# Kernel optimization log

Measured on AMD Instinct MI355X. Metric: run time of the kernel, lower is better.

## Reference

```python
import jax, jax.numpy as jnp
import numpy as np

B, N, M, K, C = 4, 8192, 2048, 32, 64
RADIUS = 0.4
XYZ_OUT = 16  # xyz_mlps spec [3, 16]


def _mlp1(x, W, b):
    # SharedMLP layer: 1x1 Conv2d + ReLU (bn=False -> bias=True)
    return jax.nn.relu(jnp.einsum('oi,bimk->bomk', W, x) + b[None, :, None, None])


def _ball_query(xyz, new_xyz):
    # xyz: [B,N,3], new_xyz: [B,M,3] -> idx [B,M,K] int32, idn [B,M,K] {0,1}
    d2 = jnp.sum((new_xyz[:, :, None, :] - xyz[:, None, :, :]) ** 2, axis=-1)  # [B,M,N]
    within = d2 < RADIUS * RADIUS
    score = jnp.where(within, jnp.arange(N, dtype=jnp.int32), jnp.int32(N))
    neg, _ = jax.lax.top_k(-score, K)  # first K in-ball indices (ascending)
    idx = -neg
    valid = idx < N
    idx = jnp.where(valid, idx, idx[..., :1])  # pad with first neighbor (CUDA ball_query semantics)
    idx = jnp.clip(idx, 0, N - 1)
    return idx, valid.astype(jnp.int32)


def setup_inputs() -> dict:
    key = jax.random.key(0)
    ks = jax.random.split(key, 16)
    s = 0.1
    return {
        'xyz': jax.random.uniform(ks[0], (B, N, 3), jnp.float32),
        'new_xyz': jax.random.uniform(ks[1], (B, M, 3), jnp.float32),
        'features': jax.random.normal(ks[2], (B, C, N), jnp.float32),
        'query_features': jax.random.normal(ks[3], (B, C, M), jnp.float32),
        # query_feats_mlps[0]: [query_ch -> neigh_ch]
        'qW': s * jax.random.normal(ks[4], (C, C), jnp.float32),
        'qb': jnp.zeros((C,), jnp.float32),
        # ad_feats_mlps[0]: [neigh_ch -> neigh_ch]
        'afW': s * jax.random.normal(ks[5], (C, C), jnp.float32),
        'afb': jnp.zeros((C,), jnp.float32),
        # ad_xyz_mlps[0]: [3 -> neigh_ch]
        'axW': s * jax.random.normal(ks[6], (C, 3), jnp.float32),
        'axb': jnp.zeros((C,), jnp.float32),
        # mlps[0]: [64 -> 64 -> 64]
        'mW1': s * jax.random.normal(ks[7], (C, C), jnp.float32),
        'mb1': jnp.zeros((C,), jnp.float32),
        'mW2': s * jax.random.normal(ks[8], (C, C), jnp.float32),
        'mb2': jnp.zeros((C,), jnp.float32),
        # xyz_mlps[0]: [3 -> 16]
        'xW': s * jax.random.normal(ks[9], (XYZ_OUT, 3), jnp.float32),
        'xb': jnp.zeros((XYZ_OUT,), jnp.float32),
    }


def reference(xyz, new_xyz, features, query_features,
              qW, qb, afW, afb, axW, axb, mW1, mb1, mW2, mb2, xW, xb):
    idx, idn = _ball_query(xyz, new_xyz)  # [B,M,K]

    # gather neighbor xyz and features
    flat = idx.reshape(B, M * K)
    g_xyz = jnp.take_along_axis(xyz, flat[:, :, None], axis=1).reshape(B, M, K, 3)
    g_xyz = (g_xyz - new_xyz[:, :, None, :]).transpose(0, 3, 1, 2)  # [B,3,M,K] relative coords
    g_feat = jnp.take_along_axis(features, flat[:, None, :], axis=2).reshape(B, C, M, K)

    idn_mask = (jnp.sum(idn, axis=2) > 0).astype(jnp.float32)[:, :, None]  # [B,M,1]
    # _idn: rows with at least one neighbor keep idn, empty rows become all-ones
    _idn = jnp.where(idn_mask > 0, idn.astype(jnp.float32), 1.0)[:, None, :, :]  # [B,1,M,K]

    q = _mlp1(query_features[:, :, :, None], qW, qb)  # [B,C,M,1]

    feats_dist = _mlp1(q - g_feat, afW, afb)          # [B,C,M,K]
    space_dist = _mlp1(g_xyz, axW, axb)               # [B,C,M,K]
    bi_edge = feats_dist * space_dist

    dist = jnp.linalg.norm(g_xyz, axis=1, keepdims=True)  # [B,1,M,K]
    dist_recip = 1.0 / (dist + 1e-8)
    dist_recip = dist_recip / _idn
    norm = jnp.sum(dist_recip, axis=3, keepdims=True)
    weights = dist_recip / norm
    weights = weights * idn_mask[:, None, :, :]  # [B,1,M,K] * [B,1,M,1]

    nf = _mlp1(_mlp1(g_feat, mW1, mb1), mW2, mb2)  # [B,C,M,K]
    nf = weights * nf * bi_edge
    nf = jnp.sum(nf, axis=3)  # [B,C,M]

    nx = _mlp1(g_xyz, xW, xb)        # [B,16,M,K]
    nx = jnp.max(nx, axis=3)         # max_pool over neighbors -> [B,16,M]

    out = jnp.concatenate([nx, nf], axis=1)  # [B,80,M]
    return (new_xyz, out)
```

## Files before the change

### kernel.cpp

```cpp
#include <hip/hip_runtime.h>

#define B_ 4
#define N_ 8192
#define M_ 2048
#define K_ 32
#define R2 0.16f

__global__ __launch_bounds__(256) void pointprep(const float* __restrict__ feats,
                                                 const float* __restrict__ afW,
                                                 const float* __restrict__ mW1, const float* __restrict__ mb1,
                                                 const float* __restrict__ mW2, const float* __restrict__ mb2,
                                                 float* __restrict__ PA,
                                                 float* __restrict__ P2) {
  __shared__ float xt[64][65];
  __shared__ float x2[64][65];
  int b = blockIdx.y, p0 = blockIdx.x * 64;
  int t = threadIdx.x, lane = t & 63;
  int g = __builtin_amdgcn_readfirstlane(t >> 6);
  const float* src = feats + ((size_t)b * 64 + g * 16) * N_ + p0 + lane;
#pragma unroll
  for (int cc = 0; cc < 16; ++cc)
    xt[g * 16 + cc][lane] = src[(size_t)cc * N_];
  __syncthreads();
  size_t orow = ((size_t)b * N_ + p0 + lane) * 64 + g * 16;
  {
    float acc[16];
#pragma unroll
    for (int cc = 0; cc < 16; ++cc) acc[cc] = 0.0f;
#pragma unroll 4
    for (int i = 0; i < 64; ++i) {
      float xv = xt[i][lane];
#pragma unroll
      for (int cc = 0; cc < 16; ++cc) acc[cc] = fmaf(afW[(g * 16 + cc) * 64 + i], xv, acc[cc]);
    }
    float4* o = (float4*)(PA + orow);
#pragma unroll
    for (int q = 0; q < 4; ++q)
      o[q] = make_float4(acc[4 * q], acc[4 * q + 1], acc[4 * q + 2], acc[4 * q + 3]);
  }
  {
    float acc[16];
#pragma unroll
    for (int cc = 0; cc < 16; ++cc) acc[cc] = mb1[g * 16 + cc];
#pragma unroll 4
    for (int i = 0; i < 64; ++i) {
      float xv = xt[i][lane];
#pragma unroll
      for (int cc = 0; cc < 16; ++cc) acc[cc] = fmaf(mW1[(g * 16 + cc) * 64 + i], xv, acc[cc]);
    }
#pragma unroll
    for (int cc = 0; cc < 16; ++cc) x2[g * 16 + cc][lane] = fmaxf(acc[cc], 0.0f);
  }
  __syncthreads();
  {
    float acc[16];
#pragma unroll
    for (int cc = 0; cc < 16; ++cc) acc[cc] = mb2[g * 16 + cc];
#pragma unroll 4
    for (int i = 0; i < 64; ++i) {
      float xv = x2[i][lane];
#pragma unroll
      for (int cc = 0; cc < 16; ++cc) acc[cc] = fmaf(mW2[(g * 16 + cc) * 64 + i], xv, acc[cc]);
    }
    float4* o = (float4*)(P2 + orow);
#pragma unroll
    for (int q = 0; q < 4; ++q)
      o[q] = make_float4(fmaxf(acc[4 * q], 0.0f), fmaxf(acc[4 * q + 1], 0.0f),
                         fmaxf(acc[4 * q + 2], 0.0f), fmaxf(acc[4 * q + 3], 0.0f));
  }
}

__global__ __launch_bounds__(256) void queryprep(const float* __restrict__ qfeat,
                                                 const float* __restrict__ qW, const float* __restrict__ qb,
                                                 const float* __restrict__ afW, const float* __restrict__ afb,
                                                 const float* __restrict__ new_xyz,
                                                 float* __restrict__ QA,
                                                 float* __restrict__ outhead) {
  __shared__ float xt[64][65];
  __shared__ float x2[64][65];
  int b = blockIdx.y, p0 = blockIdx.x * 64;
  int t = threadIdx.x, lane = t & 63;
  int g = __builtin_amdgcn_readfirstlane(t >> 6);
  const float* src = qfeat + ((size_t)b * 64 + g * 16) * M_ + p0 + lane;
#pragma unroll
  for (int cc = 0; cc < 16; ++cc)
    xt[g * 16 + cc][lane] = src[(size_t)cc * M_];
  if (t < 192) {
    size_t o = (size_t)(b * M_ + p0) * 3 + t;
    outhead[o] = new_xyz[o];
  }
  __syncthreads();
  {
    float acc[16];
#pragma unroll
    for (int cc = 0; cc < 16; ++cc) acc[cc] = qb[g * 16 + cc];
#pragma unroll 4
    for (int i = 0; i < 64; ++i) {
      float xv = xt[i][lane];
#pragma unroll
      for (int cc = 0; cc < 16; ++cc) acc[cc] = fmaf(qW[(g * 16 + cc) * 64 + i], xv, acc[cc]);
    }
#pragma unroll
    for (int cc = 0; cc < 16; ++cc) x2[g * 16 + cc][lane] = fmaxf(acc[cc], 0.0f);
  }
  __syncthreads();
  {
    float acc[16];
#pragma unroll
    for (int cc = 0; cc < 16; ++cc) acc[cc] = afb[g * 16 + cc];
#pragma unroll 4
    for (int i = 0; i < 64; ++i) {
      float xv = x2[i][lane];
#pragma unroll
      for (int cc = 0; cc < 16; ++cc) acc[cc] = fmaf(afW[(g * 16 + cc) * 64 + i], xv, acc[cc]);
    }
    float4* o = (float4*)(QA + ((size_t)b * M_ + p0 + lane) * 64 + g * 16);
#pragma unroll
    for (int q = 0; q < 4; ++q)
      o[q] = make_float4(acc[4 * q], acc[4 * q + 1], acc[4 * q + 2], acc[4 * q + 3]);
  }
}

__global__ __launch_bounds__(256) void grouper_main(
    const float* __restrict__ xyz, const float* __restrict__ new_xyz,
    const float* __restrict__ PA, const float* __restrict__ P2,
    const float* __restrict__ QA,
    const float* __restrict__ axW, const float* __restrict__ axb,
    const float* __restrict__ xW, const float* __restrict__ xb,
    float* __restrict__ out) {
  int wid = (int)((blockIdx.x * (size_t)blockDim.x + threadIdx.x) >> 6);
  int lane = threadIdx.x & 63;
  int b = wid >> 11;
  int m = wid & (M_ - 1);
  const float* qc = new_xyz + ((size_t)b * M_ + m) * 3;
  float cx = qc[0], cy = qc[1], cz = qc[2];
  const float* xbp = xyz + (size_t)b * N_ * 3;

  int idxreg = N_ - 1;
  float gxr = 0.f, gyr = 0.f, gzr = 0.f, d2r = 0.f;
  int cnt = 0;
  for (int base = 0; base < N_; base += 64) {
    int n = base + lane;
    const float* pp = xbp + 3 * n;
    float dx = pp[0] - cx, dy = pp[1] - cy, dz = pp[2] - cz;
    float d2 = dx * dx + dy * dy + dz * dz;
    bool inball = d2 < R2;
    unsigned long long mask = __ballot(inball);
    int pop = __popcll(mask);
    int before = __builtin_amdgcn_mbcnt_hi((unsigned)(mask >> 32),
                 __builtin_amdgcn_mbcnt_lo((unsigned)mask, 0));
    int pos = cnt + before;
    bool push = inball && (pos < K_);
    int dest = (push ? pos : 63) << 2;
    int rI = __builtin_amdgcn_ds_permute(dest, n);
    int rX = __builtin_amdgcn_ds_permute(dest, __float_as_int(dx));
    int rY = __builtin_amdgcn_ds_permute(dest, __float_as_int(dy));
    int rZ = __builtin_amdgcn_ds_permute(dest, __float_as_int(dz));
    int rD = __builtin_amdgcn_ds_permute(dest, __float_as_int(d2));
    int newcnt = cnt + pop;
    if ((lane >= cnt) && (lane < min(newcnt, K_))) {
      idxreg = rI; gxr = __int_as_float(rX); gyr = __int_as_float(rY);
      gzr = __int_as_float(rZ); d2r = __int_as_float(rD);
    }
    cnt = newcnt;
    if (cnt >= K_) break;
  }
  int nneigh = min(cnt, K_);
  if (nneigh == 0) {
    const float* pp = xbp + 3 * (N_ - 1);
    float dx = pp[0] - cx, dy = pp[1] - cy, dz = pp[2] - cz;
    if (lane == 0) {
      idxreg = N_ - 1; gxr = dx; gyr = dy; gzr = dz;
      d2r = dx * dx + dy * dy + dz * dz;
    }
  }
  int padn = max(nneigh, 1);
  {
    int i0 = __shfl(idxreg, 0);
    float x0 = __shfl(gxr, 0), y0 = __shfl(gyr, 0), z0 = __shfl(gzr, 0), d0 = __shfl(d2r, 0);
    if (lane >= padn) { idxreg = i0; gxr = x0; gyr = y0; gzr = z0; d2r = d0; }
  }
  float idn_mask = (nneigh > 0) ? 1.0f : 0.0f;

  size_t qb64 = ((size_t)b * M_ + m) * 64;
  float QAm = QA[qb64 + lane];
  float ax0 = axW[lane * 3 + 0], ax1 = axW[lane * 3 + 1], ax2 = axW[lane * 3 + 2];
  float axbv = axb[lane];
  float xw0 = 0.f, xw1 = 0.f, xw2 = 0.f, xbv = 0.f;
  if (lane < 16) { xw0 = xW[lane * 3 + 0]; xw1 = xW[lane * 3 + 1]; xw2 = xW[lane * 3 + 2]; xbv = xb[lane]; }

  const float* PAb = PA + (size_t)b * N_ * 64;
  const float* P2b = P2 + (size_t)b * N_ * 64;

  float accS = 0.f, Rsum = 0.f, nxmax = 0.f;
#pragma unroll 8
  for (int k = 0; k < K_; ++k) {
    int n = __builtin_amdgcn_readlane(idxreg, k);
    float gx = __int_as_float(__builtin_amdgcn_readlane(__float_as_int(gxr), k));
    float gy = __int_as_float(__builtin_amdgcn_readlane(__float_as_int(gyr), k));
    float gz = __int_as_float(__builtin_amdgcn_readlane(__float_as_int(gzr), k));
    float d2 = __int_as_float(__builtin_amdgcn_readlane(__float_as_int(d2r), k));
    float pa = PAb[(size_t)n * 64 + lane];
    float h2 = P2b[(size_t)n * 64 + lane];
    float dist = __builtin_amdgcn_sqrtf(d2);
    float r = __builtin_amdgcn_rcpf(dist + 1e-8f);
    float fd = fmaxf(QAm - pa, 0.f);
    float sd = fmaxf(fmaf(ax0, gx, fmaf(ax1, gy, fmaf(ax2, gz, axbv))), 0.f);
    accS = fmaf(r, h2 * fd * sd, accS);
    Rsum += r;
    float v = fmaxf(fmaf(xw0, gx, fmaf(xw1, gy, fmaf(xw2, gz, xbv))), 0.f);
    nxmax = fmaxf(nxmax, v);
  }
  float nf = (accS / Rsum) * idn_mask;
  float* ob = out + (size_t)b * 80 * M_;
  ob[(size_t)(16 + lane) * M_ + m] = nf;
  if (lane < 16) ob[(size_t)lane * M_ + m] = nxmax;
}

extern "C" void kernel_launch(void* const* d_in, const int* in_sizes, int n_in,
                              void* d_out, int out_size, void* d_ws, size_t ws_size,
                              hipStream_t stream) {
  const float* xyz   = (const float*)d_in[0];
  const float* nxyz  = (const float*)d_in[1];
  const float* feats = (const float*)d_in[2];
  const float* qfeat = (const float*)d_in[3];
  const float* qW  = (const float*)d_in[4];
  const float* qb  = (const float*)d_in[5];
  const float* afW = (const float*)d_in[6];
  const float* afb = (const float*)d_in[7];
  const float* axW = (const float*)d_in[8];
  const float* axb = (const float*)d_in[9];
  const float* mW1 = (const float*)d_in[10];
  const float* mb1 = (const float*)d_in[11];
  const float* mW2 = (const float*)d_in[12];
  const float* mb2 = (const float*)d_in[13];
  const float* xW  = (const float*)d_in[14];
  const float* xb  = (const float*)d_in[15];

  float* ws = (float*)d_ws;
  size_t off = 0;
  float* PA = ws + off; off += (size_t)B_ * N_ * 64;
  float* P2 = ws + off; off += (size_t)B_ * N_ * 64;
  float* QA = ws + off; off += (size_t)B_ * M_ * 64;
  if (ws_size < off * sizeof(float)) return;

  pointprep<<<dim3(N_ / 64, B_), 256, 0, stream>>>(feats, afW, mW1, mb1, mW2, mb2, PA, P2);

  float* outhead = (float*)d_out;
  queryprep<<<dim3(M_ / 64, B_), 256, 0, stream>>>(qfeat, qW, qb, afW, afb, nxyz, QA, outhead);

  float* out_main = (float*)d_out + (size_t)B_ * M_ * 3;
  grouper_main<<<B_ * M_ / 4, 256, 0, stream>>>(xyz, nxyz, PA, P2, QA,
                                                axW, axb, xW, xb, out_main);
}
```

Measured before the change: 154.3 us.

## Interleave point features, merge prep kernels, and batch neighbor gathers

```diff
diff --git a/kernel.cpp b/kernel.cpp
--- a/kernel.cpp
+++ b/kernel.cpp
@@ -6,125 +6,116 @@
 #define K_ 32
 #define R2 0.16f
 
-__global__ __launch_bounds__(256) void pointprep(const float* __restrict__ feats,
-                                                 const float* __restrict__ afW,
-                                                 const float* __restrict__ mW1, const float* __restrict__ mb1,
-                                                 const float* __restrict__ mW2, const float* __restrict__ mb2,
-                                                 float* __restrict__ PA,
-                                                 float* __restrict__ P2) {
+__device__ __forceinline__ float readlane_f(float v, int k) {
+  return __int_as_float(__builtin_amdgcn_readlane(__float_as_int(v), k));
+}
+
+__global__ __launch_bounds__(256) void prep(
+    const float* __restrict__ feats, const float* __restrict__ qfeat,
+    const float* __restrict__ qW, const float* __restrict__ qb,
+    const float* __restrict__ afW, const float* __restrict__ afb,
+    const float* __restrict__ mW1, const float* __restrict__ mb1,
+    const float* __restrict__ mW2, const float* __restrict__ mb2,
+    const float* __restrict__ new_xyz,
+    float* __restrict__ PH, float* __restrict__ QA, float* __restrict__ outhead) {
   __shared__ float xt[64][65];
   __shared__ float x2[64][65];
-  int b = blockIdx.y, p0 = blockIdx.x * 64;
+  int b = blockIdx.y;
   int t = threadIdx.x, lane = t & 63;
   int g = __builtin_amdgcn_readfirstlane(t >> 6);
-  const float* src = feats + ((size_t)b * 64 + g * 16) * N_ + p0 + lane;
-#pragma unroll
-  for (int cc = 0; cc < 16; ++cc)
-    xt[g * 16 + cc][lane] = src[(size_t)cc * N_];
-  __syncthreads();
-  size_t orow = ((size_t)b * N_ + p0 + lane) * 64 + g * 16;
-  {
-    float acc[16];
-#pragma unroll
-    for (int cc = 0; cc < 16; ++cc) acc[cc] = 0.0f;
-#pragma unroll 4
-    for (int i = 0; i < 64; ++i) {
-      float xv = xt[i][lane];
-#pragma unroll
-      for (int cc = 0; cc < 16; ++cc) acc[cc] = fmaf(afW[(g * 16 + cc) * 64 + i], xv, acc[cc]);
-    }
-    float4* o = (float4*)(PA + orow);
-#pragma unroll
-    for (int q = 0; q < 4; ++q)
-      o[q] = make_float4(acc[4 * q], acc[4 * q + 1], acc[4 * q + 2], acc[4 * q + 3]);
-  }
-  {
-    float acc[16];
-#pragma unroll
-    for (int cc = 0; cc < 16; ++cc) acc[cc] = mb1[g * 16 + cc];
-#pragma unroll 4
-    for (int i = 0; i < 64; ++i) {
-      float xv = xt[i][lane];
-#pragma unroll
-      for (int cc = 0; cc < 16; ++cc) acc[cc] = fmaf(mW1[(g * 16 + cc) * 64 + i], xv, acc[cc]);
-    }
-#pragma unroll
-    for (int cc = 0; cc < 16; ++cc) x2[g * 16 + cc][lane] = fmaxf(acc[cc], 0.0f);
-  }
-  __syncthreads();
-  {
-    float acc[16];
-#pragma unroll
-    for (int cc = 0; cc < 16; ++cc) acc[cc] = mb2[g * 16 + cc];
-#pragma unroll 4
-    for (int i = 0; i < 64; ++i) {
-      float xv = x2[i][lane];
-#pragma unroll
-      for (int cc = 0; cc < 16; ++cc) acc[cc] = fmaf(mW2[(g * 16 + cc) * 64 + i], xv, acc[cc]);
-    }
-    float4* o = (float4*)(P2 + orow);
-#pragma unroll
-    for (int q = 0; q < 4; ++q)
-      o[q] = make_float4(fmaxf(acc[4 * q], 0.0f), fmaxf(acc[4 * q + 1], 0.0f),
-                         fmaxf(acc[4 * q + 2], 0.0f), fmaxf(acc[4 * q + 3], 0.0f));
-  }
-}
-
-__global__ __launch_bounds__(256) void queryprep(const float* __restrict__ qfeat,
-                                                 const float* __restrict__ qW, const float* __restrict__ qb,
-                                                 const float* __restrict__ afW, const float* __restrict__ afb,
-                                                 const float* __restrict__ new_xyz,
-                                                 float* __restrict__ QA,
-                                                 float* __restrict__ outhead) {
-  __shared__ float xt[64][65];
-  __shared__ float x2[64][65];
-  int b = blockIdx.y, p0 = blockIdx.x * 64;
-  int t = threadIdx.x, lane = t & 63;
-  int g = __builtin_amdgcn_readfirstlane(t >> 6);
-  const float* src = qfeat + ((size_t)b * 64 + g * 16) * M_ + p0 + lane;
-#pragma unroll
-  for (int cc = 0; cc < 16; ++cc)
-    xt[g * 16 + cc][lane] = src[(size_t)cc * M_];
-  if (t < 192) {
-    size_t o = (size_t)(b * M_ + p0) * 3 + t;
-    outhead[o] = new_xyz[o];
-  }
-  __syncthreads();
-  {
-    float acc[16];
-#pragma unroll
-    for (int cc = 0; cc < 16; ++cc) acc[cc] = qb[g * 16 + cc];
-#pragma unroll 4
-    for (int i = 0; i < 64; ++i) {
-      float xv = xt[i][lane];
-#pragma unroll
-      for (int cc = 0; cc < 16; ++cc) acc[cc] = fmaf(qW[(g * 16 + cc) * 64 + i], xv, acc[cc]);
-    }
-#pragma unroll
-    for (int cc = 0; cc < 16; ++cc) x2[g * 16 + cc][lane] = fmaxf(acc[cc], 0.0f);
-  }
-  __syncthreads();
-  {
-    float acc[16];
-#pragma unroll
-    for (int cc = 0; cc < 16; ++cc) acc[cc] = afb[g * 16 + cc];
-#pragma unroll 4
-    for (int i = 0; i < 64; ++i) {
-      float xv = x2[i][lane];
-#pragma unroll
-      for (int cc = 0; cc < 16; ++cc) acc[cc] = fmaf(afW[(g * 16 + cc) * 64 + i], xv, acc[cc]);
-    }
-    float4* o = (float4*)(QA + ((size_t)b * M_ + p0 + lane) * 64 + g * 16);
-#pragma unroll
-    for (int q = 0; q < 4; ++q)
-      o[q] = make_float4(acc[4 * q], acc[4 * q + 1], acc[4 * q + 2], acc[4 * q + 3]);
+
+  if (blockIdx.x < N_ / 64) {
+    int p0 = blockIdx.x * 64;
+    const float* src = feats + ((size_t)b * 64 + g * 16) * N_ + p0 + lane;
+#pragma unroll
+    for (int cc = 0; cc < 16; ++cc) xt[g * 16 + cc][lane] = src[(size_t)cc * N_];
+    __syncthreads();
+    float pa[16];
+    {
+#pragma unroll
+      for (int cc = 0; cc < 16; ++cc) pa[cc] = 0.0f;
+#pragma unroll 4
+      for (int i = 0; i < 64; ++i) {
+        float xv = xt[i][lane];
+#pragma unroll
+        for (int cc = 0; cc < 16; ++cc) pa[cc] = fmaf(afW[(g * 16 + cc) * 64 + i], xv, pa[cc]);
+      }
+    }
+    {
+      float acc[16];
+#pragma unroll
+      for (int cc = 0; cc < 16; ++cc) acc[cc] = mb1[g * 16 + cc];
+#pragma unroll 4
+      for (int i = 0; i < 64; ++i) {
+        float xv = xt[i][lane];
+#pragma unroll
+        for (int cc = 0; cc < 16; ++cc) acc[cc] = fmaf(mW1[(g * 16 + cc) * 64 + i], xv, acc[cc]);
+      }
+#pragma unroll
+      for (int cc = 0; cc < 16; ++cc) x2[g * 16 + cc][lane] = fmaxf(acc[cc], 0.0f);
+    }
+    __syncthreads();
+    {
+      float h2[16];
+#pragma unroll
+      for (int cc = 0; cc < 16; ++cc) h2[cc] = mb2[g * 16 + cc];
+#pragma unroll 4
+      for (int i = 0; i < 64; ++i) {
+        float xv = x2[i][lane];
+#pragma unroll
+        for (int cc = 0; cc < 16; ++cc) h2[cc] = fmaf(mW2[(g * 16 + cc) * 64 + i], xv, h2[cc]);
+      }
+      float4* o = (float4*)(PH + ((size_t)b * N_ + p0 + lane) * 128 + g * 32);
+#pragma unroll
+      for (int qd = 0; qd < 8; ++qd)
+        o[qd] = make_float4(pa[2 * qd], fmaxf(h2[2 * qd], 0.0f),
+                            pa[2 * qd + 1], fmaxf(h2[2 * qd + 1], 0.0f));
+    }
+  } else {
+    int p0 = (blockIdx.x - N_ / 64) * 64;
+    const float* src = qfeat + ((size_t)b * 64 + g * 16) * M_ + p0 + lane;
+#pragma unroll
+    for (int cc = 0; cc < 16; ++cc) xt[g * 16 + cc][lane] = src[(size_t)cc * M_];
+    if (t < 192) {
+      size_t o = (size_t)(b * M_ + p0) * 3 + t;
+      outhead[o] = new_xyz[o];
+    }
+    __syncthreads();
+    {
+      float acc[16];
+#pragma unroll
+      for (int cc = 0; cc < 16; ++cc) acc[cc] = qb[g * 16 + cc];
+#pragma unroll 4
+      for (int i = 0; i < 64; ++i) {
+        float xv = xt[i][lane];
+#pragma unroll
+        for (int cc = 0; cc < 16; ++cc) acc[cc] = fmaf(qW[(g * 16 + cc) * 64 + i], xv, acc[cc]);
+      }
+#pragma unroll
+      for (int cc = 0; cc < 16; ++cc) x2[g * 16 + cc][lane] = fmaxf(acc[cc], 0.0f);
+    }
+    __syncthreads();
+    {
+      float acc[16];
+#pragma unroll
+      for (int cc = 0; cc < 16; ++cc) acc[cc] = afb[g * 16 + cc];
+#pragma unroll 4
+      for (int i = 0; i < 64; ++i) {
+        float xv = x2[i][lane];
+#pragma unroll
+        for (int cc = 0; cc < 16; ++cc) acc[cc] = fmaf(afW[(g * 16 + cc) * 64 + i], xv, acc[cc]);
+      }
+      float4* o = (float4*)(QA + ((size_t)b * M_ + p0 + lane) * 64 + g * 16);
+#pragma unroll
+      for (int q = 0; q < 4; ++q)
+        o[q] = make_float4(acc[4 * q], acc[4 * q + 1], acc[4 * q + 2], acc[4 * q + 3]);
+    }
   }
 }
 
 __global__ __launch_bounds__(256) void grouper_main(
     const float* __restrict__ xyz, const float* __restrict__ new_xyz,
-    const float* __restrict__ PA, const float* __restrict__ P2,
-    const float* __restrict__ QA,
+    const float* __restrict__ PH, const float* __restrict__ QA,
     const float* __restrict__ axW, const float* __restrict__ axb,
     const float* __restrict__ xW, const float* __restrict__ xb,
     float* __restrict__ out) {
@@ -182,6 +173,16 @@
   }
   float idn_mask = (nneigh > 0) ? 1.0f : 0.0f;
 
+  float rslot = __builtin_amdgcn_rcpf(__builtin_amdgcn_sqrtf(d2r) + 1e-8f);
+  if (nneigh > 0 && lane >= nneigh && lane < K_) rslot = __builtin_huge_valf();
+  float Rsum;
+  {
+    float s = (lane < K_) ? rslot : 0.0f;
+    s += __shfl_xor(s, 1);  s += __shfl_xor(s, 2);  s += __shfl_xor(s, 4);
+    s += __shfl_xor(s, 8);  s += __shfl_xor(s, 16); s += __shfl_xor(s, 32);
+    Rsum = s;
+  }
+
   size_t qb64 = ((size_t)b * M_ + m) * 64;
   float QAm = QA[qb64 + lane];
   float ax0 = axW[lane * 3 + 0], ax1 = axW[lane * 3 + 1], ax2 = axW[lane * 3 + 2];
@@ -189,27 +190,32 @@
   float xw0 = 0.f, xw1 = 0.f, xw2 = 0.f, xbv = 0.f;
   if (lane < 16) { xw0 = xW[lane * 3 + 0]; xw1 = xW[lane * 3 + 1]; xw2 = xW[lane * 3 + 2]; xbv = xb[lane]; }
 
-  const float* PAb = PA + (size_t)b * N_ * 64;
-  const float* P2b = P2 + (size_t)b * N_ * 64;
-
-  float accS = 0.f, Rsum = 0.f, nxmax = 0.f;
-#pragma unroll 8
-  for (int k = 0; k < K_; ++k) {
-    int n = __builtin_amdgcn_readlane(idxreg, k);
-    float gx = __int_as_float(__builtin_amdgcn_readlane(__float_as_int(gxr), k));
-    float gy = __int_as_float(__builtin_amdgcn_readlane(__float_as_int(gyr), k));
-    float gz = __int_as_float(__builtin_amdgcn_readlane(__float_as_int(gzr), k));
-    float d2 = __int_as_float(__builtin_amdgcn_readlane(__float_as_int(d2r), k));
-    float pa = PAb[(size_t)n * 64 + lane];
-    float h2 = P2b[(size_t)n * 64 + lane];
-    float dist = __builtin_amdgcn_sqrtf(d2);
-    float r = __builtin_amdgcn_rcpf(dist + 1e-8f);
-    float fd = fmaxf(QAm - pa, 0.f);
-    float sd = fmaxf(fmaf(ax0, gx, fmaf(ax1, gy, fmaf(ax2, gz, axbv))), 0.f);
-    accS = fmaf(r, h2 * fd * sd, accS);
-    Rsum += r;
-    float v = fmaxf(fmaf(xw0, gx, fmaf(xw1, gy, fmaf(xw2, gz, xbv))), 0.f);
-    nxmax = fmaxf(nxmax, v);
+  const float* PHb = PH + (size_t)b * N_ * 128;
+
+  float accS = 0.f, nxmax = 0.f;
+#pragma unroll
+  for (int kg = 0; kg < 4; ++kg) {
+    float2 v[8];
+    float gxs[8], gys[8], gzs[8], rs[8];
+#pragma unroll
+    for (int j = 0; j < 8; ++j) {
+      int k = kg * 8 + j;
+      int n = __builtin_amdgcn_readlane(idxreg, k);
+      gxs[j] = readlane_f(gxr, k);
+      gys[j] = readlane_f(gyr, k);
+      gzs[j] = readlane_f(gzr, k);
+      rs[j]  = readlane_f(rslot, k);
+      v[j] = *(const float2*)(PHb + (size_t)n * 128 + lane * 2);
+    }
+#pragma unroll
+    for (int j = 0; j < 8; ++j) {
+      float pa = v[j].x, h2 = v[j].y;
+      float fd = fmaxf(QAm - pa, 0.f);
+      float sd = fmaxf(fmaf(ax0, gxs[j], fmaf(ax1, gys[j], fmaf(ax2, gzs[j], axbv))), 0.f);
+      accS = fmaf(rs[j], h2 * fd * sd, accS);
+      float nv = fmaxf(fmaf(xw0, gxs[j], fmaf(xw1, gys[j], fmaf(xw2, gzs[j], xbv))), 0.f);
+      nxmax = fmaxf(nxmax, nv);
+    }
   }
   float nf = (accS / Rsum) * idn_mask;
   float* ob = out + (size_t)b * 80 * M_;
@@ -239,17 +245,15 @@
 
   float* ws = (float*)d_ws;
   size_t off = 0;
-  float* PA = ws + off; off += (size_t)B_ * N_ * 64;
-  float* P2 = ws + off; off += (size_t)B_ * N_ * 64;
+  float* PH = ws + off; off += (size_t)B_ * N_ * 128;
   float* QA = ws + off; off += (size_t)B_ * M_ * 64;
   if (ws_size < off * sizeof(float)) return;
 
-  pointprep<<<dim3(N_ / 64, B_), 256, 0, stream>>>(feats, afW, mW1, mb1, mW2, mb2, PA, P2);
-
   float* outhead = (float*)d_out;
-  queryprep<<<dim3(M_ / 64, B_), 256, 0, stream>>>(qfeat, qW, qb, afW, afb, nxyz, QA, outhead);
+  prep<<<dim3(N_ / 64 + M_ / 64, B_), 256, 0, stream>>>(
+      feats, qfeat, qW, qb, afW, afb, mW1, mb1, mW2, mb2, nxyz, PH, QA, outhead);
 
   float* out_main = (float*)d_out + (size_t)B_ * M_ * 3;
-  grouper_main<<<B_ * M_ / 4, 256, 0, stream>>>(xyz, nxyz, PA, P2, QA,
+  grouper_main<<<B_ * M_ / 4, 256, 0, stream>>>(xyz, nxyz, PH, QA,
                                                 axW, axb, xW, xb, out_main);
 }
```

Result: faster. 136.7 us (-11.4%).
